# Performance work log

Measured on AMD Instinct MI355X. Metric: run time of the kernel, lower is better.

The kernel has to match this reference:

```python
import jax, jax.numpy as jnp
import numpy as np

H, D, BETA = 12, 64, 1.0
EPS = 1e-8


def setup_inputs() -> dict:
    key = jax.random.key(0)
    k1, k2 = jax.random.split(key)
    n, dim = 1024, H * D
    x = jax.random.normal(k1, (n, dim), dtype=jnp.float32)
    mask = jnp.ones((n, n), dtype=bool)
    W_qk = jax.random.normal(k2, (2 * H * D, dim), dtype=jnp.float32) / np.sqrt(dim).astype(np.float32)
    return {"x": x, "mask": mask, "W_qk": W_qk}


def _free_energy_heads(xh, mask, W_qk):
    # xh: (H, n, D) unit-norm token vectors per head -> per-head free energy (H,)
    n = xh.shape[1]
    xf = jnp.transpose(xh, (1, 0, 2)).reshape(n, H * D)      # 'h n d -> n (h d)'
    qk = xf @ W_qk.T                                          # (n, 2*H*D), Linear no-bias
    q, k = jnp.split(qk, 2, axis=-1)
    q = jnp.transpose(q.reshape(n, H, D), (1, 0, 2))          # (H, n, D)
    k = jnp.transpose(k.reshape(n, H, D), (1, 0, 2))
    sim = jnp.einsum('hid,hjd->hij', q, k)                    # (H, n, n)
    sim = jnp.where(mask, sim, jnp.finfo(sim.dtype).min)
    J = jax.scipy.special.logsumexp(sim, axis=-1)             # (H, n)
    # t* = root of quadratic: beta*t^2 + (-0.5 - 2 beta J) t + (beta J^2 + 0.5 J - 0.25 beta |x|^2)
    hn = jnp.sum(xh * xh, axis=-1)                            # (H, n), |x_i|^2
    b = -0.5 - 2.0 * BETA * J
    c = BETA * J ** 2 + 0.5 * J - 0.25 * BETA * hn
    t = (-b + jnp.sqrt(b * b - 4.0 * BETA * c)) / (2.0 * BETA)
    v = t - J                                                 # (H, n)
    inv_v = 1.0 / jnp.clip(v, EPS, jnp.finfo(v.dtype).max)    # safe_reciprocal
    phi = (BETA * jnp.sum(t, axis=-1)
           - 0.5 * jnp.sum(jnp.log(v + EPS), axis=-1)
           + 0.25 * BETA * jnp.sum(hn * inv_v, axis=-1))      # (H,)
    log_Z = -0.5 * n * (1.0 + jnp.log(2.0 * BETA)) + phi
    return -log_Z / BETA                                      # (H,)


def reference(x, mask, W_qk):
    n = x.shape[0]
    xh = jnp.transpose(x.reshape(n, H, D), (1, 0, 2))         # (H, n, D)
    xh = xh / jnp.linalg.norm(xh, axis=-1, keepdims=True)
    jac = jax.jacrev(lambda xs: _free_energy_heads(xs, mask, W_qk))(xh)  # (H, H, n, D)
    diag = jnp.diagonal(jac)                                  # (n, D, H): dF_h/dx_h only
    out = jnp.transpose(diag, (0, 2, 1)).reshape(n, H * D)    # 'n d h -> n (h d)'
    return -out
```

## Files before the change

kernel.cpp:

```cpp
#include <hip/hip_runtime.h>
#include <hip/hip_cooperative_groups.h>
#include <cstdint>

namespace cg = cooperative_groups;

#define NTOK 1024
#define NH   12
#define HD   64
#define DIM  768
#define QKD  1536

static constexpr float C2G = 0.61803398874989485f;

typedef __bf16 bf16x8 __attribute__((ext_vector_type(8)));
typedef __bf16 bf16x4 __attribute__((ext_vector_type(4)));
typedef float  f32x4  __attribute__((ext_vector_type(4)));

#define MFMA16(a, b, c) __builtin_amdgcn_mfma_f32_16x16x32_bf16((a), (b), (c), 0, 0, 0)

#define FRAG(S, outer, ks) (*(const bf16x8*)&S[(outer) + (l & 15)][(ks) * 32 + (l >> 4) * 8])

__device__ __forceinline__ bf16x4 cvt4(float4 v, float s) {
  bf16x4 o;
  o[0] = (__bf16)(v.x * s); o[1] = (__bf16)(v.y * s);
  o[2] = (__bf16)(v.z * s); o[3] = (__bf16)(v.w * s);
  return o;
}

__global__ __launch_bounds__(256) void fused_k(
    const float* __restrict__ x, const float* __restrict__ W,
    float* __restrict__ xf, __bf16* __restrict__ WT,
    __bf16* __restrict__ qkb, __bf16* __restrict__ qkT,
    float* __restrict__ part_k, float* __restrict__ part_z,
    float* __restrict__ out) {
  cg::grid_group grid = cg::this_grid();
  __shared__ __align__(16) __bf16 T[6][64][72];
  __shared__ float Zs[64];
  const int b = blockIdx.x, t = threadIdx.x, l = t & 63, w = t >> 6;
  const int R = (w >> 1) * 32, Cc = (w & 1) * 32;
  const int srow = t >> 2, scol = (t & 3) * 16;

  {
    int m0 = (b & 15) * 64, n0 = (b >> 4) * 64;
    bool wxf = (b >> 4) == 0;

    if (b < 24) {
      float (*Ws)[65] = (float(*)[65])T;
      int h = b % NH, p = b / NH;
      int rowbase = p * DIM + h * HD;
#pragma unroll
      for (int rr = 0; rr < 16; ++rr) {
        int row = rr * 4 + (t >> 6), col = t & 63;
        Ws[row][col] = W[(size_t)(rowbase + row) * DIM + h * HD + col];
      }
      __syncthreads();
      __bf16* dst = WT + ((size_t)p * NH + h) * HD * HD;
#pragma unroll
      for (int rr = 0; rr < 16; ++rr) {
        int dlt = rr * 4 + (t >> 6), d = t & 63;
        dst[dlt * HD + d] = (__bf16)Ws[d][dlt];
      }
      __syncthreads();
    }

    const float* xrow = x + (size_t)(m0 + srow) * DIM + scol;
    const float* wrow = W + (size_t)(n0 + srow) * DIM + scol;
    float4 a4[4], b4[4];
#pragma unroll
    for (int q = 0; q < 4; ++q) {
      a4[q] = *(const float4*)(xrow + q * 4);
      b4[q] = *(const float4*)(wrow + q * 4);
    }
    f32x4 acc[2][2] = {};
    for (int kt = 0; kt < 12; ++kt) {
      int buf = kt & 1;
      float ss = 0.f;
#pragma unroll
      for (int q = 0; q < 4; ++q)
        ss += a4[q].x * a4[q].x + a4[q].y * a4[q].y + a4[q].z * a4[q].z + a4[q].w * a4[q].w;
      ss += __shfl_xor(ss, 1);
      ss += __shfl_xor(ss, 2);
      float inv = rsqrtf(ss);
#pragma unroll
      for (int q = 0; q < 4; ++q) {
        *(bf16x4*)&T[buf][srow][scol + q * 4]     = cvt4(a4[q], inv);
        *(bf16x4*)&T[2 + buf][srow][scol + q * 4] = cvt4(b4[q], 1.0f);
        if (wxf) {
          float4 av = make_float4(a4[q].x * inv, a4[q].y * inv, a4[q].z * inv, a4[q].w * inv);
          *(float4*)(xf + (size_t)(m0 + srow) * DIM + kt * 64 + scol + q * 4) = av;
        }
      }
      if (kt < 11) {
#pragma unroll
        for (int q = 0; q < 4; ++q) {
          a4[q] = *(const float4*)(xrow + (kt + 1) * 64 + q * 4);
          b4[q] = *(const float4*)(wrow + (kt + 1) * 64 + q * 4);
        }
      }
      __syncthreads();
#pragma unroll
      for (int ks = 0; ks < 2; ++ks) {
        bf16x8 af[2], bf[2];
#pragma unroll
        for (int mf = 0; mf < 2; ++mf) af[mf] = FRAG(T[buf], R + mf * 16, ks);
#pragma unroll
        for (int nf = 0; nf < 2; ++nf) bf[nf] = FRAG(T[2 + buf], Cc + nf * 16, ks);
#pragma unroll
        for (int mf = 0; mf < 2; ++mf)
#pragma unroll
          for (int nf = 0; nf < 2; ++nf) acc[mf][nf] = MFMA16(af[mf], bf[nf], acc[mf][nf]);
      }
    }
#pragma unroll
    for (int mf = 0; mf < 2; ++mf)
#pragma unroll
      for (int nf = 0; nf < 2; ++nf)
#pragma unroll
        for (int r = 0; r < 4; ++r) {
          int row = R + mf * 16 + (l >> 4) * 4 + r;
          int col = Cc + nf * 16 + (l & 15);
          __bf16 v = (__bf16)acc[mf][nf][r];
          T[4][row][col] = v;
          T[5][col][row] = v;
        }
    __syncthreads();
    *(uint4*)(qkb + (size_t)(m0 + srow) * QKD + n0 + scol)     = *(const uint4*)&T[4][srow][scol];
    *(uint4*)(qkb + (size_t)(m0 + srow) * QKD + n0 + scol + 8) = *(const uint4*)&T[4][srow][scol + 8];
    *(uint4*)(qkT + (size_t)(n0 + srow) * NTOK + m0 + scol)     = *(const uint4*)&T[5][srow][scol];
    *(uint4*)(qkT + (size_t)(n0 + srow) * NTOK + m0 + scol + 8) = *(const uint4*)&T[5][srow][scol + 8];
  }
  __threadfence();
  grid.sync();

  {
    int h = b >> 5, rem = b & 31;
    int i0 = (rem >> 1) * 64;
    int jt0 = (rem & 1) * 8;
    const __bf16* kbase  = qkb + DIM + h * HD;
    const __bf16* ktbase = qkT + (size_t)(DIM + h * HD + srow) * NTOK;
    *(uint4*)&T[0][srow][scol]     = *(const uint4*)(qkb + (size_t)(i0 + srow) * QKD + h * HD + scol);
    *(uint4*)&T[0][srow][scol + 8] = *(const uint4*)(qkb + (size_t)(i0 + srow) * QKD + h * HD + scol + 8);
    if (t < 64) Zs[t] = 0.f;
    uint4 kA = *(const uint4*)(kbase + (size_t)(jt0 * 64 + srow) * QKD + scol);
    uint4 kB = *(const uint4*)(kbase + (size_t)(jt0 * 64 + srow) * QKD + scol + 8);
    uint4 tA = *(const uint4*)(ktbase + jt0 * 64 + scol);
    uint4 tB = *(const uint4*)(ktbase + jt0 * 64 + scol + 8);
    f32x4 facc[2][2] = {};
    float zacc[8] = {0.f, 0.f, 0.f, 0.f, 0.f, 0.f, 0.f, 0.f};
    for (int jt = jt0; jt < jt0 + 8; ++jt) {
      int buf = jt & 1;
      *(uint4*)&T[1 + buf][srow][scol]     = kA;
      *(uint4*)&T[1 + buf][srow][scol + 8] = kB;
      *(uint4*)&T[3 + buf][srow][scol]     = tA;
      *(uint4*)&T[3 + buf][srow][scol + 8] = tB;
      if (jt < jt0 + 7) {
        int j0 = (jt + 1) * 64;
        kA = *(const uint4*)(kbase + (size_t)(j0 + srow) * QKD + scol);
        kB = *(const uint4*)(kbase + (size_t)(j0 + srow) * QKD + scol + 8);
        tA = *(const uint4*)(ktbase + j0 + scol);
        tB = *(const uint4*)(ktbase + j0 + scol + 8);
      }
      __syncthreads();
      f32x4 sacc[2][2] = {};
#pragma unroll
      for (int ks = 0; ks < 2; ++ks) {
        bf16x8 af[2], bf[2];
#pragma unroll
        for (int mf = 0; mf < 2; ++mf) af[mf] = FRAG(T[0], R + mf * 16, ks);
#pragma unroll
        for (int nf = 0; nf < 2; ++nf) bf[nf] = FRAG(T[1 + buf], Cc + nf * 16, ks);
#pragma unroll
        for (int mf = 0; mf < 2; ++mf)
#pragma unroll
          for (int nf = 0; nf < 2; ++nf) sacc[mf][nf] = MFMA16(af[mf], bf[nf], sacc[mf][nf]);
      }
#pragma unroll
      for (int mf = 0; mf < 2; ++mf)
#pragma unroll
        for (int r = 0; r < 4; ++r) {
          float e0 = __expf(sacc[mf][0][r]);
          float e1 = __expf(sacc[mf][1][r]);
          zacc[mf * 4 + r] += e0 + e1;
          int row = R + mf * 16 + (l >> 4) * 4 + r;
          T[5][row][Cc + (l & 15)]      = (__bf16)e0;
          T[5][row][Cc + 16 + (l & 15)] = (__bf16)e1;
        }
      __syncthreads();
#pragma unroll
      for (int ks = 0; ks < 2; ++ks) {
        bf16x8 af[2], bf[2];
#pragma unroll
        for (int mf = 0; mf < 2; ++mf) af[mf] = FRAG(T[5], R + mf * 16, ks);
#pragma unroll
        for (int nf = 0; nf < 2; ++nf) bf[nf] = FRAG(T[3 + buf], Cc + nf * 16, ks);
#pragma unroll
        for (int mf = 0; mf < 2; ++mf)
#pragma unroll
          for (int nf = 0; nf < 2; ++nf) facc[mf][nf] = MFMA16(af[mf], bf[nf], facc[mf][nf]);
      }
    }
    float* pk = part_k + (size_t)b * 4096;
#pragma unroll
    for (int mf = 0; mf < 2; ++mf)
#pragma unroll
      for (int nf = 0; nf < 2; ++nf)
#pragma unroll
        for (int r = 0; r < 4; ++r) {
          int row = R + mf * 16 + (l >> 4) * 4 + r;
          int col = Cc + nf * 16 + (l & 15);
          pk[row * 64 + col] = facc[mf][nf][r];
        }
#pragma unroll
    for (int zi = 0; zi < 8; ++zi) {
      float z = zacc[zi];
      z += __shfl_xor(z, 1); z += __shfl_xor(z, 2);
      z += __shfl_xor(z, 4); z += __shfl_xor(z, 8);
      if ((l & 15) == 0) {
        int row = R + (zi >> 2) * 16 + (l >> 4) * 4 + (zi & 3);
        atomicAdd(&Zs[row], z);
      }
    }
    __syncthreads();
    if (t < 64) part_z[(size_t)b * 64 + t] = Zs[t];
  }
  __threadfence();
  grid.sync();

  if (b < 192) {
    int h = b >> 4, jidx = b & 15, j0 = jidx * 64;
    const __bf16* qbase  = qkb + h * HD;
    const __bf16* qtbase = qkT + (size_t)(h * HD + srow) * NTOK;
    const float*  pz     = part_z + (size_t)h * 2048;
    *(uint4*)&T[0][srow][scol]     = *(const uint4*)(qkb + (size_t)(j0 + srow) * QKD + DIM + h * HD + scol);
    *(uint4*)&T[0][srow][scol + 8] = *(const uint4*)(qkb + (size_t)(j0 + srow) * QKD + DIM + h * HD + scol + 8);
    uint4 qA = *(const uint4*)(qbase + (size_t)srow * QKD + scol);
    uint4 qB = *(const uint4*)(qbase + (size_t)srow * QKD + scol + 8);
    uint4 tA = *(const uint4*)(qtbase + scol);
    uint4 tB = *(const uint4*)(qtbase + scol + 8);
    f32x4 facc[2][2] = {};
    for (int it = 0; it < 16; ++it) {
      int buf = it & 1;
      *(uint4*)&T[1 + buf][srow][scol]     = qA;
      *(uint4*)&T[1 + buf][srow][scol + 8] = qB;
      *(uint4*)&T[3 + buf][srow][scol]     = tA;
      *(uint4*)&T[3 + buf][srow][scol + 8] = tB;
      if (it < 15) {
        int i0 = (it + 1) * 64;
        qA = *(const uint4*)(qbase + (size_t)(i0 + srow) * QKD + scol);
        qB = *(const uint4*)(qbase + (size_t)(i0 + srow) * QKD + scol + 8);
        tA = *(const uint4*)(qtbase + i0 + scol);
        tB = *(const uint4*)(qtbase + i0 + scol + 8);
      }
      __syncthreads();
      f32x4 sacc[2][2] = {};
#pragma unroll
      for (int ks = 0; ks < 2; ++ks) {
        bf16x8 af[2], bf[2];
#pragma unroll
        for (int mf = 0; mf < 2; ++mf) af[mf] = FRAG(T[0], R + mf * 16, ks);
#pragma unroll
        for (int nf = 0; nf < 2; ++nf) bf[nf] = FRAG(T[1 + buf], Cc + nf * 16, ks);
#pragma unroll
        for (int mf = 0; mf < 2; ++mf)
#pragma unroll
          for (int nf = 0; nf < 2; ++nf) sacc[mf][nf] = MFMA16(af[mf], bf[nf], sacc[mf][nf]);
      }
      float iz0 = 1.0f / (pz[it * 128 + Cc + (l & 15)]      + pz[it * 128 + 64 + Cc + (l & 15)]);
      float iz1 = 1.0f / (pz[it * 128 + Cc + 16 + (l & 15)] + pz[it * 128 + 64 + Cc + 16 + (l & 15)]);
#pragma unroll
      for (int mf = 0; mf < 2; ++mf)
#pragma unroll
        for (int r = 0; r < 4; ++r) {
          float e0 = __expf(sacc[mf][0][r]) * iz0;
          float e1 = __expf(sacc[mf][1][r]) * iz1;
          int row = R + mf * 16 + (l >> 4) * 4 + r;
          T[5][row][Cc + (l & 15)]      = (__bf16)e0;
          T[5][row][Cc + 16 + (l & 15)] = (__bf16)e1;
        }
      __syncthreads();
#pragma unroll
      for (int ks = 0; ks < 2; ++ks) {
        bf16x8 af[2], bf[2];
#pragma unroll
        for (int mf = 0; mf < 2; ++mf) af[mf] = FRAG(T[5], R + mf * 16, ks);
#pragma unroll
        for (int nf = 0; nf < 2; ++nf) bf[nf] = FRAG(T[3 + buf], Cc + nf * 16, ks);
#pragma unroll
        for (int mf = 0; mf < 2; ++mf)
#pragma unroll
          for (int nf = 0; nf < 2; ++nf) facc[mf][nf] = MFMA16(af[mf], bf[nf], facc[mf][nf]);
      }
    }
    __syncthreads();
    const float* pk  = part_k + (size_t)(h * 32 + jidx * 2) * 4096;
    const float* pzr = part_z + (size_t)(h * 32 + jidx * 2) * 64;
#pragma unroll
    for (int mf = 0; mf < 2; ++mf)
#pragma unroll
      for (int r = 0; r < 4; ++r) {
        int row = R + mf * 16 + (l >> 4) * 4 + r;
        float iz = 1.0f / (pzr[row] + pzr[64 + row]);
#pragma unroll
        for (int nf = 0; nf < 2; ++nf) {
          int col = Cc + nf * 16 + (l & 15);
          int off = row * 64 + col;
          T[0][row][col] = (__bf16)((pk[off] + pk[4096 + off]) * iz);
          T[1][row][col] = (__bf16)facc[mf][nf][r];
        }
      }
    const __bf16* wq = WT + (size_t)h * HD * HD;
    const __bf16* wk = WT + ((size_t)NH + h) * HD * HD;
    *(uint4*)&T[2][srow][scol]     = *(const uint4*)(wq + (size_t)srow * HD + scol);
    *(uint4*)&T[2][srow][scol + 8] = *(const uint4*)(wq + (size_t)srow * HD + scol + 8);
    *(uint4*)&T[3][srow][scol]     = *(const uint4*)(wk + (size_t)srow * HD + scol);
    *(uint4*)&T[3][srow][scol + 8] = *(const uint4*)(wk + (size_t)srow * HD + scol + 8);
    __syncthreads();
    f32x4 acc2[2][2] = {};
#pragma unroll
    for (int ks = 0; ks < 2; ++ks) {
      bf16x8 af[2], bf[2];
#pragma unroll
      for (int mf = 0; mf < 2; ++mf) af[mf] = FRAG(T[0], R + mf * 16, ks);
#pragma unroll
      for (int nf = 0; nf < 2; ++nf) bf[nf] = FRAG(T[2], Cc + nf * 16, ks);
#pragma unroll
      for (int mf = 0; mf < 2; ++mf)
#pragma unroll
        for (int nf = 0; nf < 2; ++nf) acc2[mf][nf] = MFMA16(af[mf], bf[nf], acc2[mf][nf]);
    }
#pragma unroll
    for (int ks = 0; ks < 2; ++ks) {
      bf16x8 af[2], bf[2];
#pragma unroll
      for (int mf = 0; mf < 2; ++mf) af[mf] = FRAG(T[1], R + mf * 16, ks);
#pragma unroll
      for (int nf = 0; nf < 2; ++nf) bf[nf] = FRAG(T[3], Cc + nf * 16, ks);
#pragma unroll
      for (int mf = 0; mf < 2; ++mf)
#pragma unroll
        for (int nf = 0; nf < 2; ++nf) acc2[mf][nf] = MFMA16(af[mf], bf[nf], acc2[mf][nf]);
    }
#pragma unroll
    for (int mf = 0; mf < 2; ++mf)
#pragma unroll
      for (int nf = 0; nf < 2; ++nf)
#pragma unroll
        for (int r = 0; r < 4; ++r) {
          int row = j0 + R + mf * 16 + (l >> 4) * 4 + r;
          int col = h * HD + Cc + nf * 16 + (l & 15);
          size_t idx = (size_t)row * DIM + col;
          out[idx] = acc2[mf][nf][r] + C2G * xf[idx];
        }
  }
}

__global__ __launch_bounds__(256) void prep_k(const float* __restrict__ x,
                                              const float* __restrict__ W,
                                              float* __restrict__ xf,
                                              __bf16* __restrict__ xhb,
                                              __bf16* __restrict__ Wb,
                                              __bf16* __restrict__ WT,
                                              float* __restrict__ Zg) {
  __shared__ float Ws[64][65];
  int b = blockIdx.x, t = threadIdx.x;
  if (b < 3072) {
    int gid  = b * 4 + (t >> 6);
    int lane = t & 63;
    int i = gid / NH, h = gid - i * NH;
    size_t idx = (size_t)i * DIM + h * HD + lane;
    float v = x[idx];
    float ss = v * v;
#pragma unroll
    for (int m = 1; m < 64; m <<= 1) ss += __shfl_xor(ss, m);
    float r = v * rsqrtf(ss);
    xf[idx] = r;
    xhb[idx] = (__bf16)r;
  } else if (b < 4224) {
    int tg = (b - 3072) * 256 + t;
    float4 v = ((const float4*)W)[tg];
    bf16x4 o;
    o[0] = (__bf16)v.x; o[1] = (__bf16)v.y; o[2] = (__bf16)v.z; o[3] = (__bf16)v.w;
    *(bf16x4*)(Wb + (size_t)tg * 4) = o;
  } else if (b < 4248) {
    int bb = b - 4224;
    int h = bb % NH, p = bb / NH;
    int rowbase = p * DIM + h * HD;
#pragma unroll
    for (int rr = 0; rr < 16; ++rr) {
      int row = rr * 4 + (t >> 6), col = t & 63;
      Ws[row][col] = W[(size_t)(rowbase + row) * DIM + h * HD + col];
    }
    __syncthreads();
    __bf16* dst = WT + ((size_t)p * NH + h) * HD * HD;
#pragma unroll
    for (int rr = 0; rr < 16; ++rr) {
      int dlt = rr * 4 + (t >> 6), d = t & 63;
      dst[dlt * HD + d] = (__bf16)Ws[d][dlt];
    }
  } else {
    int zz = b - 4248;
    ((float4*)Zg)[zz * 256 + t] = make_float4(0.f, 0.f, 0.f, 0.f);
  }
}

__global__ __launch_bounds__(256) void gemm_dual_k(const __bf16* __restrict__ A,
                                                   const __bf16* __restrict__ Bt,
                                                   __bf16* __restrict__ qkb,
                                                   __bf16* __restrict__ qkT) {
  __shared__ __align__(16) __bf16 As[2][64][72], Bs[2][64][72];
  int m0 = blockIdx.x * 64, n0 = blockIdx.y * 64;
  int t = threadIdx.x, l = t & 63, w = t >> 6;
  int R = (w >> 1) * 32, Cc = (w & 1) * 32;
  int srow = t >> 2, scol = (t & 3) * 16;
  uint4 aA = *(const uint4*)(A  + (size_t)(m0 + srow) * DIM + scol);
  uint4 aB = *(const uint4*)(A  + (size_t)(m0 + srow) * DIM + scol + 8);
  uint4 bA = *(const uint4*)(Bt + (size_t)(n0 + srow) * DIM + scol);
  uint4 bB = *(const uint4*)(Bt + (size_t)(n0 + srow) * DIM + scol + 8);
  f32x4 acc[2][2] = {};
  for (int kt = 0; kt < 12; ++kt) {
    int buf = kt & 1;
    *(uint4*)&As[buf][srow][scol]     = aA;
    *(uint4*)&As[buf][srow][scol + 8] = aB;
    *(uint4*)&Bs[buf][srow][scol]     = bA;
    *(uint4*)&Bs[buf][srow][scol + 8] = bB;
    if (kt < 11) {
      int k0 = (kt + 1) * 64;
      aA = *(const uint4*)(A  + (size_t)(m0 + srow) * DIM + k0 + scol);
      aB = *(const uint4*)(A  + (size_t)(m0 + srow) * DIM + k0 + scol + 8);
      bA = *(const uint4*)(Bt + (size_t)(n0 + srow) * DIM + k0 + scol);
      bB = *(const uint4*)(Bt + (size_t)(n0 + srow) * DIM + k0 + scol + 8);
    }
    __syncthreads();
#pragma unroll
    for (int ks = 0; ks < 2; ++ks) {
      bf16x8 af[2], bf[2];
#pragma unroll
      for (int mf = 0; mf < 2; ++mf) af[mf] = FRAG(As[buf], R + mf * 16, ks);
#pragma unroll
      for (int nf = 0; nf < 2; ++nf) bf[nf] = FRAG(Bs[buf], Cc + nf * 16, ks);
#pragma unroll
      for (int mf = 0; mf < 2; ++mf)
#pragma unroll
        for (int nf = 0; nf < 2; ++nf) acc[mf][nf] = MFMA16(af[mf], bf[nf], acc[mf][nf]);
    }
  }
#pragma unroll
  for (int mf = 0; mf < 2; ++mf)
#pragma unroll
    for (int nf = 0; nf < 2; ++nf) {
      int rowb = m0 + R + mf * 16 + (l >> 4) * 4;
      int col  = n0 + Cc + nf * 16 + (l & 15);
      bf16x4 o4;
#pragma unroll
      for (int r = 0; r < 4; ++r) {
        __bf16 v = (__bf16)acc[mf][nf][r];
        o4[r] = v;
        qkb[(size_t)(rowb + r) * QKD + col] = v;
      }
      *(bf16x4*)(qkT + (size_t)col * NTOK + rowb) = o4;
    }
}

__global__ __launch_bounds__(256) void kbarp_k(const __bf16* __restrict__ qkb,
                                               const __bf16* __restrict__ qkT,
                                               float* __restrict__ part_k,
                                               float* __restrict__ Zg) {
  __shared__ __align__(16) __bf16 Qs[64][72], Ks[2][64][72], KTs[2][64][72], Es[64][72];
  int u = blockIdx.x;
  int h = u >> 5, rem = u & 31;
  int i0 = (rem >> 1) * 64;
  int jt0 = (rem & 1) * 8;
  int t = threadIdx.x, l = t & 63, w = t >> 6;
  int R = (w >> 1) * 32, Cc = (w & 1) * 32;
  int srow = t >> 2, scol = (t & 3) * 16;
  const __bf16* kbase  = qkb + DIM + h * HD;
  const __bf16* ktbase = qkT + (size_t)(DIM + h * HD + srow) * NTOK;
  *(uint4*)&Qs[srow][scol]     = *(const uint4*)(qkb + (size_t)(i0 + srow) * QKD + h * HD + scol);
  *(uint4*)&Qs[srow][scol + 8] = *(const uint4*)(qkb + (size_t)(i0 + srow) * QKD + h * HD + scol + 8);
  uint4 kA = *(const uint4*)(kbase + (size_t)(jt0 * 64 + srow) * QKD + scol);
  uint4 kB = *(const uint4*)(kbase + (size_t)(jt0 * 64 + srow) * QKD + scol + 8);
  uint4 tA = *(const uint4*)(ktbase + jt0 * 64 + scol);
  uint4 tB = *(const uint4*)(ktbase + jt0 * 64 + scol + 8);
  f32x4 facc[2][2] = {};
  float zacc[8] = {0.f, 0.f, 0.f, 0.f, 0.f, 0.f, 0.f, 0.f};
  for (int jt = jt0; jt < jt0 + 8; ++jt) {
    int buf = jt & 1;
    *(uint4*)&Ks[buf][srow][scol]      = kA;
    *(uint4*)&Ks[buf][srow][scol + 8]  = kB;
    *(uint4*)&KTs[buf][srow][scol]     = tA;
    *(uint4*)&KTs[buf][srow][scol + 8] = tB;
    if (jt < jt0 + 7) {
      int j0 = (jt + 1) * 64;
      kA = *(const uint4*)(kbase + (size_t)(j0 + srow) * QKD + scol);
      kB = *(const uint4*)(kbase + (size_t)(j0 + srow) * QKD + scol + 8);
      tA = *(const uint4*)(ktbase + j0 + scol);
      tB = *(const uint4*)(ktbase + j0 + scol + 8);
    }
    __syncthreads();
    f32x4 sacc[2][2] = {};
#pragma unroll
    for (int ks = 0; ks < 2; ++ks) {
      bf16x8 af[2], bf[2];
#pragma unroll
      for (int mf = 0; mf < 2; ++mf) af[mf] = FRAG(Qs, R + mf * 16, ks);
#pragma unroll
      for (int nf = 0; nf < 2; ++nf) bf[nf] = FRAG(Ks[buf], Cc + nf * 16, ks);
#pragma unroll
      for (int mf = 0; mf < 2; ++mf)
#pragma unroll
        for (int nf = 0; nf < 2; ++nf) sacc[mf][nf] = MFMA16(af[mf], bf[nf], sacc[mf][nf]);
    }
#pragma unroll
    for (int mf = 0; mf < 2; ++mf)
#pragma unroll
      for (int r = 0; r < 4; ++r) {
        float e0 = __expf(sacc[mf][0][r]);
        float e1 = __expf(sacc[mf][1][r]);
        zacc[mf * 4 + r] += e0 + e1;
        int row = R + mf * 16 + (l >> 4) * 4 + r;
        Es[row][Cc + (l & 15)]      = (__bf16)e0;
        Es[row][Cc + 16 + (l & 15)] = (__bf16)e1;
      }
    __syncthreads();
#pragma unroll
    for (int ks = 0; ks < 2; ++ks) {
      bf16x8 af[2], bf[2];
#pragma unroll
      for (int mf = 0; mf < 2; ++mf) af[mf] = FRAG(Es, R + mf * 16, ks);
#pragma unroll
      for (int nf = 0; nf < 2; ++nf) bf[nf] = FRAG(KTs[buf], Cc + nf * 16, ks);
#pragma unroll
      for (int mf = 0; mf < 2; ++mf)
#pragma unroll
        for (int nf = 0; nf < 2; ++nf) facc[mf][nf] = MFMA16(af[mf], bf[nf], facc[mf][nf]);
    }
  }
  float* pk = part_k + (size_t)u * 4096;
#pragma unroll
  for (int mf = 0; mf < 2; ++mf)
#pragma unroll
    for (int nf = 0; nf < 2; ++nf)
#pragma unroll
      for (int r = 0; r < 4; ++r) {
        int row = R + mf * 16 + (l >> 4) * 4 + r;
        int col = Cc + nf * 16 + (l & 15);
        pk[row * 64 + col] = facc[mf][nf][r];
      }
#pragma unroll
  for (int zi = 0; zi < 8; ++zi) {
    float z = zacc[zi];
    z += __shfl_xor(z, 1); z += __shfl_xor(z, 2);
    z += __shfl_xor(z, 4); z += __shfl_xor(z, 8);
    if ((l & 15) == 0) {
      int row = R + (zi >> 2) * 16 + (l >> 4) * 4 + (zi & 3);
      atomicAdd(&Zg[(size_t)h * NTOK + i0 + row], z);
    }
  }
}

__global__ __launch_bounds__(256) void qbarp_k(const __bf16* __restrict__ qkb,
                                               const __bf16* __restrict__ qkT,
                                               const float* __restrict__ Zg,
                                               float* __restrict__ part_q) {
  __shared__ __align__(16) __bf16 Ks[64][72], Qs[2][64][72], QTs[2][64][72], Es[64][72];
  int u = blockIdx.x;
  int h = u >> 5, rem = u & 31;
  int j0 = (rem >> 1) * 64;
  int it0 = (rem & 1) * 8;
  int t = threadIdx.x, l = t & 63, w = t >> 6;
  int R = (w >> 1) * 32, Cc = (w & 1) * 32;
  int srow = t >> 2, scol = (t & 3) * 16;
  const __bf16* qbase  = qkb + h * HD;
  const __bf16* qtbase = qkT + (size_t)(h * HD + srow) * NTOK;
  const float*  zb     = Zg + (size_t)h * NTOK;
  *(uint4*)&Ks[srow][scol]     = *(const uint4*)(qkb + (size_t)(j0 + srow) * QKD + DIM + h * HD + scol);
  *(uint4*)&Ks[srow][scol + 8] = *(const uint4*)(qkb + (size_t)(j0 + srow) * QKD + DIM + h * HD + scol + 8);
  uint4 qA = *(const uint4*)(qbase + (size_t)(it0 * 64 + srow) * QKD + scol);
  uint4 qB = *(const uint4*)(qbase + (size_t)(it0 * 64 + srow) * QKD + scol + 8);
  uint4 tA = *(const uint4*)(qtbase + it0 * 64 + scol);
  uint4 tB = *(const uint4*)(qtbase + it0 * 64 + scol + 8);
  f32x4 facc[2][2] = {};
  for (int it = it0; it < it0 + 8; ++it) {
    int buf = it & 1;
    *(uint4*)&Qs[buf][srow][scol]      = qA;
    *(uint4*)&Qs[buf][srow][scol + 8]  = qB;
    *(uint4*)&QTs[buf][srow][scol]     = tA;
    *(uint4*)&QTs[buf][srow][scol + 8] = tB;
    if (it < it0 + 7) {
      int i0 = (it + 1) * 64;
      qA = *(const uint4*)(qbase + (size_t)(i0 + srow) * QKD + scol);
      qB = *(const uint4*)(qbase + (size_t)(i0 + srow) * QKD + scol + 8);
      tA = *(const uint4*)(qtbase + i0 + scol);
      tB = *(const uint4*)(qtbase + i0 + scol + 8);
    }
    __syncthreads();
    f32x4 sacc[2][2] = {};
#pragma unroll
    for (int ks = 0; ks < 2; ++ks) {
      bf16x8 af[2], bf[2];
#pragma unroll
      for (int mf = 0; mf < 2; ++mf) af[mf] = FRAG(Ks, R + mf * 16, ks);
#pragma unroll
      for (int nf = 0; nf < 2; ++nf) bf[nf] = FRAG(Qs[buf], Cc + nf * 16, ks);
#pragma unroll
      for (int mf = 0; mf < 2; ++mf)
#pragma unroll
        for (int nf = 0; nf < 2; ++nf) sacc[mf][nf] = MFMA16(af[mf], bf[nf], sacc[mf][nf]);
    }
    float iz0 = 1.0f / zb[it * 64 + Cc + (l & 15)];
    float iz1 = 1.0f / zb[it * 64 + Cc + 16 + (l & 15)];
#pragma unroll
    for (int mf = 0; mf < 2; ++mf)
#pragma unroll
      for (int r = 0; r < 4; ++r) {
        float e0 = __expf(sacc[mf][0][r]) * iz0;
        float e1 = __expf(sacc[mf][1][r]) * iz1;
        int row = R + mf * 16 + (l >> 4) * 4 + r;
        Es[row][Cc + (l & 15)]      = (__bf16)e0;
        Es[row][Cc + 16 + (l & 15)] = (__bf16)e1;
      }
    __syncthreads();
#pragma unroll
    for (int ks = 0; ks < 2; ++ks) {
      bf16x8 af[2], bf[2];
#pragma unroll
      for (int mf = 0; mf < 2; ++mf) af[mf] = FRAG(Es, R + mf * 16, ks);
#pragma unroll
      for (int nf = 0; nf < 2; ++nf) bf[nf] = FRAG(QTs[buf], Cc + nf * 16, ks);
#pragma unroll
      for (int mf = 0; mf < 2; ++mf)
#pragma unroll
        for (int nf = 0; nf < 2; ++nf) facc[mf][nf] = MFMA16(af[mf], bf[nf], facc[mf][nf]);
    }
  }
  float* pq = part_q + (size_t)u * 4096;
#pragma unroll
  for (int mf = 0; mf < 2; ++mf)
#pragma unroll
    for (int nf = 0; nf < 2; ++nf)
#pragma unroll
      for (int r = 0; r < 4; ++r) {
        int row = R + mf * 16 + (l >> 4) * 4 + r;
        int col = Cc + nf * 16 + (l & 15);
        pq[row * 64 + col] = facc[mf][nf][r];
      }
}

__global__ __launch_bounds__(256) void final2_k(const float* __restrict__ part_k,
                                                const float* __restrict__ part_q,
                                                const float* __restrict__ Zg,
                                                const __bf16* __restrict__ WT,
                                                const float* __restrict__ xf,
                                                float* __restrict__ out) {
  __shared__ __align__(16) __bf16 Ka[64][72], Qa[64][72], WqS[64][72], WkS[64][72];
  int u = blockIdx.x;
  int h = u >> 4, jidx = u & 15, j0 = jidx * 64;
  int t = threadIdx.x, l = t & 63, w = t >> 6;
  int R = (w >> 1) * 32, Cc = (w & 1) * 32;
  int srow = t >> 2, scol = (t & 3) * 16;
  const float* pk = part_k + ((size_t)(h * 32 + jidx * 2)) * 4096;
  const float* pq = part_q + ((size_t)(h * 32 + jidx * 2)) * 4096;
#pragma unroll
  for (int mf = 0; mf < 2; ++mf)
#pragma unroll
    for (int r = 0; r < 4; ++r) {
      int row = R + mf * 16 + (l >> 4) * 4 + r;
      float iz = 1.0f / Zg[(size_t)h * NTOK + j0 + row];
#pragma unroll
      for (int nf = 0; nf < 2; ++nf) {
        int col = Cc + nf * 16 + (l & 15);
        int off = row * 64 + col;
        Ka[row][col] = (__bf16)((pk[off] + pk[4096 + off]) * iz);
        Qa[row][col] = (__bf16)(pq[off] + pq[4096 + off]);
      }
    }
  const __bf16* wq = WT + (size_t)h * HD * HD;
  const __bf16* wk = WT + ((size_t)NH + h) * HD * HD;
  *(uint4*)&WqS[srow][scol]     = *(const uint4*)(wq + (size_t)srow * HD + scol);
  *(uint4*)&WqS[srow][scol + 8] = *(const uint4*)(wq + (size_t)srow * HD + scol + 8);
  *(uint4*)&WkS[srow][scol]     = *(const uint4*)(wk + (size_t)srow * HD + scol);
  *(uint4*)&WkS[srow][scol + 8] = *(const uint4*)(wk + (size_t)srow * HD + scol + 8);
  __syncthreads();
  f32x4 acc[2][2] = {};
#pragma unroll
  for (int ks = 0; ks < 2; ++ks) {
    bf16x8 af[2], bf[2];
#pragma unroll
    for (int mf = 0; mf < 2; ++mf) af[mf] = FRAG(Ka, R + mf * 16, ks);
#pragma unroll
    for (int nf = 0; nf < 2; ++nf) bf[nf] = FRAG(WqS, Cc + nf * 16, ks);
#pragma unroll
    for (int mf = 0; mf < 2; ++mf)
#pragma unroll
      for (int nf = 0; nf < 2; ++nf) acc[mf][nf] = MFMA16(af[mf], bf[nf], acc[mf][nf]);
  }
#pragma unroll
  for (int ks = 0; ks < 2; ++ks) {
    bf16x8 af[2], bf[2];
#pragma unroll
    for (int mf = 0; mf < 2; ++mf) af[mf] = FRAG(Qa, R + mf * 16, ks);
#pragma unroll
    for (int nf = 0; nf < 2; ++nf) bf[nf] = FRAG(WkS, Cc + nf * 16, ks);
#pragma unroll
    for (int mf = 0; mf < 2; ++mf)
#pragma unroll
      for (int nf = 0; nf < 2; ++nf) acc[mf][nf] = MFMA16(af[mf], bf[nf], acc[mf][nf]);
  }
#pragma unroll
  for (int mf = 0; mf < 2; ++mf)
#pragma unroll
    for (int nf = 0; nf < 2; ++nf)
#pragma unroll
      for (int r = 0; r < 4; ++r) {
        int row = j0 + R + mf * 16 + (l >> 4) * 4 + r;
        int col = h * HD + Cc + nf * 16 + (l & 15);
        size_t idx = (size_t)row * DIM + col;
        out[idx] = acc[mf][nf][r] + C2G * xf[idx];
      }
}

extern "C" void kernel_launch(void* const* d_in, const int* in_sizes, int n_in,
                              void* d_out, int out_size, void* d_ws, size_t ws_size,
                              hipStream_t stream) {
  const float* x = (const float*)d_in[0];
  const float* W = (const float*)d_in[2];
  float* out = (float*)d_out;

  float* wsf = (float*)d_ws;
  size_t off = 0;
  float* xf     = wsf + off; off += (size_t)NTOK * DIM;
  float* Zg     = wsf + off; off += (size_t)NH * NTOK;
  float* part_k = wsf + off; off += (size_t)384 * 4096;
  float* part_q = wsf + off; off += (size_t)384 * 4096;
  float* part_z = wsf + off; off += (size_t)384 * 64;
  __bf16* wsb = (__bf16*)(wsf + off);
  size_t boff = 0;
  __bf16* xhb = wsb + boff; boff += (size_t)NTOK * DIM;
  __bf16* Wb  = wsb + boff; boff += (size_t)QKD * DIM;
  __bf16* WT  = wsb + boff; boff += (size_t)2 * NH * HD * HD;
  __bf16* qkb = wsb + boff; boff += (size_t)NTOK * QKD;
  __bf16* qkT = wsb + boff; boff += (size_t)QKD * NTOK;

  int maxb = 0;
  hipOccupancyMaxActiveBlocksPerMultiprocessor(&maxb, fused_k, 256, 0);
  int dev = 0, ncu = 0;
  hipGetDevice(&dev);
  hipDeviceGetAttribute(&ncu, hipDeviceAttributeMultiprocessorCount, dev);
  bool coop = (maxb > 0 && ncu > 0 && (long)maxb * ncu >= 384);

  if (coop) {
    void* args[] = {(void*)&x, (void*)&W, (void*)&xf, (void*)&WT,
                    (void*)&qkb, (void*)&qkT, (void*)&part_k, (void*)&part_z,
                    (void*)&out};
    hipLaunchCooperativeKernel(fused_k, dim3(384), dim3(256), args, 0, stream);
  } else {
    prep_k<<<dim3(4260), dim3(256), 0, stream>>>(x, W, xf, xhb, Wb, WT, Zg);
    gemm_dual_k<<<dim3(16, 24), dim3(256), 0, stream>>>(xhb, Wb, qkb, qkT);
    kbarp_k<<<dim3(384), dim3(256), 0, stream>>>(qkb, qkT, part_k, Zg);
    qbarp_k<<<dim3(384), dim3(256), 0, stream>>>(qkb, qkT, Zg, part_q);
    final2_k<<<dim3(192), dim3(256), 0, stream>>>(part_k, part_q, Zg, WT, xf, out);
  }
}
```

Baseline: 50.54 us.

## Double cooperative grid to 768 blocks with finer work split and extra reduction phase

Raises the cooperative grid from 384 to 768 blocks with launch bounds targeting 4 blocks per CU. The QK GEMM now uses 64x32 tiles, and the k-bar and q-bar phases each split their loops into quarters. The q-bar phase now runs on all blocks, writes partials to part_q, and a new grid sync plus final phase reduces the four partials. Shared memory shrinks by dropping double buffering in the attention loops, which adds a __syncthreads per iteration. The extra grid barrier and partial-buffer traffic are traded for more parallelism on the 256-CU device.

Measured after the change: 50.25 us, median of 2. No clear change (-0.6%).

```diff
diff --git a/kernel.cpp b/kernel.cpp
--- a/kernel.cpp
+++ b/kernel.cpp
@@ -27,23 +27,20 @@
   return o;
 }
 
-__global__ __launch_bounds__(256) void fused_k(
+__global__ __launch_bounds__(256, 4) void fused_k(
     const float* __restrict__ x, const float* __restrict__ W,
     float* __restrict__ xf, __bf16* __restrict__ WT,
     __bf16* __restrict__ qkb, __bf16* __restrict__ qkT,
-    float* __restrict__ part_k, float* __restrict__ part_z,
-    float* __restrict__ out) {
+    float* __restrict__ part_k, float* __restrict__ part_q,
+    float* __restrict__ part_z, float* __restrict__ out) {
   cg::grid_group grid = cg::this_grid();
-  __shared__ __align__(16) __bf16 T[6][64][72];
+  __shared__ __align__(16) __bf16 T[4][64][72];
   __shared__ float Zs[64];
   const int b = blockIdx.x, t = threadIdx.x, l = t & 63, w = t >> 6;
   const int R = (w >> 1) * 32, Cc = (w & 1) * 32;
   const int srow = t >> 2, scol = (t & 3) * 16;
 
   {
-    int m0 = (b & 15) * 64, n0 = (b >> 4) * 64;
-    bool wxf = (b >> 4) == 0;
-
     if (b < 24) {
       float (*Ws)[65] = (float(*)[65])T;
       int h = b % NH, p = b / NH;
@@ -63,15 +60,19 @@
       __syncthreads();
     }
 
-    const float* xrow = x + (size_t)(m0 + srow) * DIM + scol;
-    const float* wrow = W + (size_t)(n0 + srow) * DIM + scol;
-    float4 a4[4], b4[4];
-#pragma unroll
-    for (int q = 0; q < 4; ++q) {
-      a4[q] = *(const float4*)(xrow + q * 4);
-      b4[q] = *(const float4*)(wrow + q * 4);
-    }
-    f32x4 acc[2][2] = {};
+    int i0 = (b & 15) * 64, o0 = (b >> 4) * 32;
+    bool wxf = (b >> 4) == 0;
+    int R2 = w * 16;
+    int srow2 = t >> 3, scol2 = (t & 7) * 8;
+    __bf16 (*Bs)[72] = (__bf16(*)[72])&T[2][0][0];
+    const float* xrow = x + (size_t)(i0 + srow) * DIM + scol;
+    const float* wrow = W + (size_t)(o0 + srow2) * DIM + scol2;
+    float4 a4[4], b4[2];
+#pragma unroll
+    for (int q = 0; q < 4; ++q) a4[q] = *(const float4*)(xrow + q * 4);
+#pragma unroll
+    for (int q = 0; q < 2; ++q) b4[q] = *(const float4*)(wrow + q * 4);
+    f32x4 acc[2] = {};
     for (int kt = 0; kt < 12; ++kt) {
       int buf = kt & 1;
       float ss = 0.f;
@@ -83,59 +84,56 @@
       float inv = rsqrtf(ss);
 #pragma unroll
       for (int q = 0; q < 4; ++q) {
-        *(bf16x4*)&T[buf][srow][scol + q * 4]     = cvt4(a4[q], inv);
-        *(bf16x4*)&T[2 + buf][srow][scol + q * 4] = cvt4(b4[q], 1.0f);
+        *(bf16x4*)&T[buf][srow][scol + q * 4] = cvt4(a4[q], inv);
         if (wxf) {
           float4 av = make_float4(a4[q].x * inv, a4[q].y * inv, a4[q].z * inv, a4[q].w * inv);
-          *(float4*)(xf + (size_t)(m0 + srow) * DIM + kt * 64 + scol + q * 4) = av;
+          *(float4*)(xf + (size_t)(i0 + srow) * DIM + kt * 64 + scol + q * 4) = av;
         }
       }
+#pragma unroll
+      for (int q = 0; q < 2; ++q)
+        *(bf16x4*)&Bs[buf * 32 + srow2][scol2 + q * 4] = cvt4(b4[q], 1.0f);
       if (kt < 11) {
 #pragma unroll
-        for (int q = 0; q < 4; ++q) {
-          a4[q] = *(const float4*)(xrow + (kt + 1) * 64 + q * 4);
-          b4[q] = *(const float4*)(wrow + (kt + 1) * 64 + q * 4);
+        for (int q = 0; q < 4; ++q) a4[q] = *(const float4*)(xrow + (kt + 1) * 64 + q * 4);
+#pragma unroll
+        for (int q = 0; q < 2; ++q) b4[q] = *(const float4*)(wrow + (kt + 1) * 64 + q * 4);
+      }
+      __syncthreads();
+#pragma unroll
+      for (int ks = 0; ks < 2; ++ks) {
+        bf16x8 af = *(const bf16x8*)&T[buf][R2 + (l & 15)][ks * 32 + (l >> 4) * 8];
+#pragma unroll
+        for (int nf = 0; nf < 2; ++nf) {
+          bf16x8 bfr = *(const bf16x8*)&Bs[buf * 32 + nf * 16 + (l & 15)][ks * 32 + (l >> 4) * 8];
+          acc[nf] = MFMA16(af, bfr, acc[nf]);
         }
       }
-      __syncthreads();
-#pragma unroll
-      for (int ks = 0; ks < 2; ++ks) {
-        bf16x8 af[2], bf[2];
-#pragma unroll
-        for (int mf = 0; mf < 2; ++mf) af[mf] = FRAG(T[buf], R + mf * 16, ks);
-#pragma unroll
-        for (int nf = 0; nf < 2; ++nf) bf[nf] = FRAG(T[2 + buf], Cc + nf * 16, ks);
-#pragma unroll
-        for (int mf = 0; mf < 2; ++mf)
-#pragma unroll
-          for (int nf = 0; nf < 2; ++nf) acc[mf][nf] = MFMA16(af[mf], bf[nf], acc[mf][nf]);
-      }
-    }
-#pragma unroll
-    for (int mf = 0; mf < 2; ++mf)
-#pragma unroll
-      for (int nf = 0; nf < 2; ++nf)
-#pragma unroll
-        for (int r = 0; r < 4; ++r) {
-          int row = R + mf * 16 + (l >> 4) * 4 + r;
-          int col = Cc + nf * 16 + (l & 15);
-          __bf16 v = (__bf16)acc[mf][nf][r];
-          T[4][row][col] = v;
-          T[5][col][row] = v;
-        }
-    __syncthreads();
-    *(uint4*)(qkb + (size_t)(m0 + srow) * QKD + n0 + scol)     = *(const uint4*)&T[4][srow][scol];
-    *(uint4*)(qkb + (size_t)(m0 + srow) * QKD + n0 + scol + 8) = *(const uint4*)&T[4][srow][scol + 8];
-    *(uint4*)(qkT + (size_t)(n0 + srow) * NTOK + m0 + scol)     = *(const uint4*)&T[5][srow][scol];
-    *(uint4*)(qkT + (size_t)(n0 + srow) * NTOK + m0 + scol + 8) = *(const uint4*)&T[5][srow][scol + 8];
+    }
+    __bf16 (*T4)[40] = (__bf16(*)[40])&T[0][0][0];
+    __bf16 (*T5)[72] = (__bf16(*)[72])&T[3][0][0];
+#pragma unroll
+    for (int nf = 0; nf < 2; ++nf) {
+      bf16x4 p;
+#pragma unroll
+      for (int r = 0; r < 4; ++r) {
+        __bf16 v = (__bf16)acc[nf][r];
+        T4[R2 + (l >> 4) * 4 + r][nf * 16 + (l & 15)] = v;
+        p[r] = v;
+      }
+      *(bf16x4*)&T5[nf * 16 + (l & 15)][R2 + (l >> 4) * 4] = p;
+    }
+    __syncthreads();
+    *(uint4*)(qkb + (size_t)(i0 + (t >> 2)) * QKD + o0 + (t & 3) * 8) = *(const uint4*)&T4[t >> 2][(t & 3) * 8];
+    *(uint4*)(qkT + (size_t)(o0 + (t >> 3)) * NTOK + i0 + (t & 7) * 8) = *(const uint4*)&T5[t >> 3][(t & 7) * 8];
   }
   __threadfence();
   grid.sync();
 
   {
-    int h = b >> 5, rem = b & 31;
-    int i0 = (rem >> 1) * 64;
-    int jt0 = (rem & 1) * 8;
+    int h = b >> 6, rem = b & 63;
+    int i0 = (rem >> 2) * 64;
+    int jt0 = (rem & 3) * 4;
     const __bf16* kbase  = qkb + DIM + h * HD;
     const __bf16* ktbase = qkT + (size_t)(DIM + h * HD + srow) * NTOK;
     *(uint4*)&T[0][srow][scol]     = *(const uint4*)(qkb + (size_t)(i0 + srow) * QKD + h * HD + scol);
@@ -147,13 +145,13 @@
     uint4 tB = *(const uint4*)(ktbase + jt0 * 64 + scol + 8);
     f32x4 facc[2][2] = {};
     float zacc[8] = {0.f, 0.f, 0.f, 0.f, 0.f, 0.f, 0.f, 0.f};
-    for (int jt = jt0; jt < jt0 + 8; ++jt) {
-      int buf = jt & 1;
-      *(uint4*)&T[1 + buf][srow][scol]     = kA;
-      *(uint4*)&T[1 + buf][srow][scol + 8] = kB;
-      *(uint4*)&T[3 + buf][srow][scol]     = tA;
-      *(uint4*)&T[3 + buf][srow][scol + 8] = tB;
-      if (jt < jt0 + 7) {
+    for (int jt = jt0; jt < jt0 + 4; ++jt) {
+      __syncthreads();
+      *(uint4*)&T[1][srow][scol]     = kA;
+      *(uint4*)&T[1][srow][scol + 8] = kB;
+      *(uint4*)&T[2][srow][scol]     = tA;
+      *(uint4*)&T[2][srow][scol + 8] = tB;
+      if (jt < jt0 + 3) {
         int j0 = (jt + 1) * 64;
         kA = *(const uint4*)(kbase + (size_t)(j0 + srow) * QKD + scol);
         kB = *(const uint4*)(kbase + (size_t)(j0 + srow) * QKD + scol + 8);
@@ -168,7 +166,7 @@
 #pragma unroll
         for (int mf = 0; mf < 2; ++mf) af[mf] = FRAG(T[0], R + mf * 16, ks);
 #pragma unroll
-        for (int nf = 0; nf < 2; ++nf) bf[nf] = FRAG(T[1 + buf], Cc + nf * 16, ks);
+        for (int nf = 0; nf < 2; ++nf) bf[nf] = FRAG(T[1], Cc + nf * 16, ks);
 #pragma unroll
         for (int mf = 0; mf < 2; ++mf)
 #pragma unroll
@@ -182,17 +180,17 @@
           float e1 = __expf(sacc[mf][1][r]);
           zacc[mf * 4 + r] += e0 + e1;
           int row = R + mf * 16 + (l >> 4) * 4 + r;
-          T[5][row][Cc + (l & 15)]      = (__bf16)e0;
-          T[5][row][Cc + 16 + (l & 15)] = (__bf16)e1;
+          T[3][row][Cc + (l & 15)]      = (__bf16)e0;
+          T[3][row][Cc + 16 + (l & 15)] = (__bf16)e1;
         }
       __syncthreads();
 #pragma unroll
       for (int ks = 0; ks < 2; ++ks) {
         bf16x8 af[2], bf[2];
 #pragma unroll
-        for (int mf = 0; mf < 2; ++mf) af[mf] = FRAG(T[5], R + mf * 16, ks);
-#pragma unroll
-        for (int nf = 0; nf < 2; ++nf) bf[nf] = FRAG(T[3 + buf], Cc + nf * 16, ks);
+        for (int mf = 0; mf < 2; ++mf) af[mf] = FRAG(T[3], R + mf * 16, ks);
+#pragma unroll
+        for (int nf = 0; nf < 2; ++nf) bf[nf] = FRAG(T[2], Cc + nf * 16, ks);
 #pragma unroll
         for (int mf = 0; mf < 2; ++mf)
 #pragma unroll
@@ -226,25 +224,30 @@
   __threadfence();
   grid.sync();
 
-  if (b < 192) {
-    int h = b >> 4, jidx = b & 15, j0 = jidx * 64;
+  {
+    int h = b >> 6, rem = b & 63;
+    int j0 = (rem >> 2) * 64;
+    int it0 = (rem & 3) * 4;
     const __bf16* qbase  = qkb + h * HD;
     const __bf16* qtbase = qkT + (size_t)(h * HD + srow) * NTOK;
-    const float*  pz     = part_z + (size_t)h * 2048;
     *(uint4*)&T[0][srow][scol]     = *(const uint4*)(qkb + (size_t)(j0 + srow) * QKD + DIM + h * HD + scol);
     *(uint4*)&T[0][srow][scol + 8] = *(const uint4*)(qkb + (size_t)(j0 + srow) * QKD + DIM + h * HD + scol + 8);
-    uint4 qA = *(const uint4*)(qbase + (size_t)srow * QKD + scol);
-    uint4 qB = *(const uint4*)(qbase + (size_t)srow * QKD + scol + 8);
-    uint4 tA = *(const uint4*)(qtbase + scol);
-    uint4 tB = *(const uint4*)(qtbase + scol + 8);
+    uint4 qA = *(const uint4*)(qbase + (size_t)(it0 * 64 + srow) * QKD + scol);
+    uint4 qB = *(const uint4*)(qbase + (size_t)(it0 * 64 + srow) * QKD + scol + 8);
+    uint4 tA = *(const uint4*)(qtbase + it0 * 64 + scol);
+    uint4 tB = *(const uint4*)(qtbase + it0 * 64 + scol + 8);
     f32x4 facc[2][2] = {};
-    for (int it = 0; it < 16; ++it) {
-      int buf = it & 1;
-      *(uint4*)&T[1 + buf][srow][scol]     = qA;
-      *(uint4*)&T[1 + buf][srow][scol + 8] = qB;
-      *(uint4*)&T[3 + buf][srow][scol]     = tA;
-      *(uint4*)&T[3 + buf][srow][scol + 8] = tB;
-      if (it < 15) {
+    for (int it = it0; it < it0 + 4; ++it) {
+      __syncthreads();
+      *(uint4*)&T[1][srow][scol]     = qA;
+      *(uint4*)&T[1][srow][scol + 8] = qB;
+      *(uint4*)&T[2][srow][scol]     = tA;
+      *(uint4*)&T[2][srow][scol + 8] = tB;
+      if (t < 64) {
+        const float* pz = part_z + (size_t)(h * 64 + it * 4) * 64;
+        Zs[t] = 1.0f / (pz[t] + pz[64 + t] + pz[128 + t] + pz[192 + t]);
+      }
+      if (it < it0 + 3) {
         int i0 = (it + 1) * 64;
         qA = *(const uint4*)(qbase + (size_t)(i0 + srow) * QKD + scol);
         qB = *(const uint4*)(qbase + (size_t)(i0 + srow) * QKD + scol + 8);
@@ -259,14 +262,14 @@
 #pragma unroll
         for (int mf = 0; mf < 2; ++mf) af[mf] = FRAG(T[0], R + mf * 16, ks);
 #pragma unroll
-        for (int nf = 0; nf < 2; ++nf) bf[nf] = FRAG(T[1 + buf], Cc + nf * 16, ks);
+        for (int nf = 0; nf < 2; ++nf) bf[nf] = FRAG(T[1], Cc + nf * 16, ks);
 #pragma unroll
         for (int mf = 0; mf < 2; ++mf)
 #pragma unroll
           for (int nf = 0; nf < 2; ++nf) sacc[mf][nf] = MFMA16(af[mf], bf[nf], sacc[mf][nf]);
       }
-      float iz0 = 1.0f / (pz[it * 128 + Cc + (l & 15)]      + pz[it * 128 + 64 + Cc + (l & 15)]);
-      float iz1 = 1.0f / (pz[it * 128 + Cc + 16 + (l & 15)] + pz[it * 128 + 64 + Cc + 16 + (l & 15)]);
+      float iz0 = Zs[Cc + (l & 15)];
+      float iz1 = Zs[Cc + 16 + (l & 15)];
 #pragma unroll
       for (int mf = 0; mf < 2; ++mf)
 #pragma unroll
@@ -274,46 +277,68 @@
           float e0 = __expf(sacc[mf][0][r]) * iz0;
           float e1 = __expf(sacc[mf][1][r]) * iz1;
           int row = R + mf * 16 + (l >> 4) * 4 + r;
-          T[5][row][Cc + (l & 15)]      = (__bf16)e0;
-          T[5][row][Cc + 16 + (l & 15)] = (__bf16)e1;
+          T[3][row][Cc + (l & 15)]      = (__bf16)e0;
+          T[3][row][Cc + 16 + (l & 15)] = (__bf16)e1;
         }
       __syncthreads();
 #pragma unroll
       for (int ks = 0; ks < 2; ++ks) {
         bf16x8 af[2], bf[2];
 #pragma unroll
-        for (int mf = 0; mf < 2; ++mf) af[mf] = FRAG(T[5], R + mf * 16, ks);
-#pragma unroll
-        for (int nf = 0; nf < 2; ++nf) bf[nf] = FRAG(T[3 + buf], Cc + nf * 16, ks);
+        for (int mf = 0; mf < 2; ++mf) af[mf] = FRAG(T[3], R + mf * 16, ks);
+#pragma unroll
+        for (int nf = 0; nf < 2; ++nf) bf[nf] = FRAG(T[2], Cc + nf * 16, ks);
 #pragma unroll
         for (int mf = 0; mf < 2; ++mf)
 #pragma unroll
           for (int nf = 0; nf < 2; ++nf) facc[mf][nf] = MFMA16(af[mf], bf[nf], facc[mf][nf]);
       }
     }
-    __syncthreads();
-    const float* pk  = part_k + (size_t)(h * 32 + jidx * 2) * 4096;
-    const float* pzr = part_z + (size_t)(h * 32 + jidx * 2) * 64;
+    float* pq = part_q + (size_t)b * 4096;
 #pragma unroll
     for (int mf = 0; mf < 2; ++mf)
 #pragma unroll
-      for (int r = 0; r < 4; ++r) {
-        int row = R + mf * 16 + (l >> 4) * 4 + r;
-        float iz = 1.0f / (pzr[row] + pzr[64 + row]);
-#pragma unroll
-        for (int nf = 0; nf < 2; ++nf) {
+      for (int nf = 0; nf < 2; ++nf)
+#pragma unroll
+        for (int r = 0; r < 4; ++r) {
+          int row = R + mf * 16 + (l >> 4) * 4 + r;
           int col = Cc + nf * 16 + (l & 15);
-          int off = row * 64 + col;
-          T[0][row][col] = (__bf16)((pk[off] + pk[4096 + off]) * iz);
-          T[1][row][col] = (__bf16)facc[mf][nf][r];
+          pq[row * 64 + col] = facc[mf][nf][r];
         }
-      }
+  }
+  __threadfence();
+  grid.sync();
+
+  if (b < 192) {
+    int h = b >> 4, m = b & 15, j0 = m * 64;
+    const float* pk = part_k + (size_t)(h * 64 + m * 4) * 4096;
+    const float* pq = part_q + (size_t)(h * 64 + m * 4) * 4096;
+    const float* pz = part_z + (size_t)(h * 64 + m * 4) * 64;
+    if (t < 64)
+      Zs[t] = 1.0f / (pz[t] + pz[64 + t] + pz[128 + t] + pz[192 + t]);
     const __bf16* wq = WT + (size_t)h * HD * HD;
     const __bf16* wk = WT + ((size_t)NH + h) * HD * HD;
     *(uint4*)&T[2][srow][scol]     = *(const uint4*)(wq + (size_t)srow * HD + scol);
     *(uint4*)&T[2][srow][scol + 8] = *(const uint4*)(wq + (size_t)srow * HD + scol + 8);
     *(uint4*)&T[3][srow][scol]     = *(const uint4*)(wk + (size_t)srow * HD + scol);
     *(uint4*)&T[3][srow][scol + 8] = *(const uint4*)(wk + (size_t)srow * HD + scol + 8);
+    __syncthreads();
+#pragma unroll
+    for (int mf = 0; mf < 2; ++mf)
+#pragma unroll
+      for (int r = 0; r < 4; ++r) {
+        int row = R + mf * 16 + (l >> 4) * 4 + r;
+        float iz = Zs[row];
+#pragma unroll
+        for (int nf = 0; nf < 2; ++nf) {
+          int col = Cc + nf * 16 + (l & 15);
+          int off = row * 64 + col;
+          float kv = pk[off] + pk[4096 + off] + pk[8192 + off] + pk[12288 + off];
+          float qv = pq[off] + pq[4096 + off] + pq[8192 + off] + pq[12288 + off];
+          T[0][row][col] = (__bf16)(kv * iz);
+          T[1][row][col] = (__bf16)qv;
+        }
+      }
     __syncthreads();
     f32x4 acc2[2][2] = {};
 #pragma unroll
@@ -730,9 +755,9 @@
   size_t off = 0;
   float* xf     = wsf + off; off += (size_t)NTOK * DIM;
   float* Zg     = wsf + off; off += (size_t)NH * NTOK;
-  float* part_k = wsf + off; off += (size_t)384 * 4096;
-  float* part_q = wsf + off; off += (size_t)384 * 4096;
-  float* part_z = wsf + off; off += (size_t)384 * 64;
+  float* part_k = wsf + off; off += (size_t)768 * 4096;
+  float* part_q = wsf + off; off += (size_t)768 * 4096;
+  float* part_z = wsf + off; off += (size_t)768 * 64;
   __bf16* wsb = (__bf16*)(wsf + off);
   size_t boff = 0;
   __bf16* xhb = wsb + boff; boff += (size_t)NTOK * DIM;
@@ -746,13 +771,13 @@
   int dev = 0, ncu = 0;
   hipGetDevice(&dev);
   hipDeviceGetAttribute(&ncu, hipDeviceAttributeMultiprocessorCount, dev);
-  bool coop = (maxb > 0 && ncu > 0 && (long)maxb * ncu >= 384);
+  bool coop = (maxb > 0 && ncu > 0 && (long)maxb * ncu >= 768);
 
   if (coop) {
     void* args[] = {(void*)&x, (void*)&W, (void*)&xf, (void*)&WT,
-                    (void*)&qkb, (void*)&qkT, (void*)&part_k, (void*)&part_z,
-                    (void*)&out};
-    hipLaunchCooperativeKernel(fused_k, dim3(384), dim3(256), args, 0, stream);
+                    (void*)&qkb, (void*)&qkT, (void*)&part_k, (void*)&part_q,
+                    (void*)&part_z, (void*)&out};
+    hipLaunchCooperativeKernel(fused_k, dim3(768), dim3(256), args, 0, stream);
   } else {
     prep_k<<<dim3(4260), dim3(256), 0, stream>>>(x, W, xf, xhb, Wb, WT, Zg);
     gemm_dual_k<<<dim3(16, 24), dim3(256), 0, stream>>>(xhb, Wb, qkb, qkT);
```
